# Kernel tuning notes

Measured on AMD Instinct MI355X. Metric: run time of the kernel, lower is better.

## Reference

```python
import jax, jax.numpy as jnp
import numpy as np

NT, NTRACES, NCH = 4096, 1024, 4


def setup_inputs() -> dict:
    key = jax.random.key(0)
    k1, k2 = jax.random.split(key)
    x = jax.random.normal(k1, (NT, NTRACES, NCH), dtype=jnp.float32)
    y = jax.random.normal(k2, (NT, NTRACES, NCH), dtype=jnp.float32)
    return {"x": x, "y": y}


def _quantiles(qs, cws, values):
    # quantile function of the discrete measure (values, weights with cumsum cws)
    # evaluated at cumulative-mass levels qs (POT solver_1d convention:
    # searchsorted side='left', clipped to valid index range).
    idx = jnp.clip(jnp.searchsorted(cws, qs, side="left"), 0, values.shape[0] - 1)
    return values[idx]


def _emd2_1d(xv, yv, w):
    # 1D EMD^2 (sqeuclidean ground metric, as in ot.emd2_1d defaults) between
    # atoms at positions xv with weights w and atoms at yv with weights w.
    ix = jnp.argsort(xv)
    iy = jnp.argsort(yv)
    xs, ys = xv[ix], yv[iy]            # sorted positions
    ca = jnp.cumsum(w[ix])             # cumulative source mass
    cb = jnp.cumsum(w[iy])             # cumulative target mass (equal total)
    qs = jnp.sort(jnp.concatenate([ca, cb]))  # merged mass breakpoints, (2*nt,)
    qx = _quantiles(qs, ca, xs)
    qy = _quantiles(qs, cb, ys)
    delta = jnp.diff(qs, prepend=0.0)  # mass in each segment
    return jnp.sum(delta * (qx - qy) ** 2)


def _sinkhorn_pair(xv, yv, t):
    # faithful to Sinkhorn._sinkhorn: clamp(min=0) -> cumsum -> divide by the
    # SUM of the cumsum (note: not the last element) -> 1D EMD with positions
    # (xv, yv) and weights t = arange(nt)  [positional args of ot.emd2_1d].
    xv = jnp.cumsum(jnp.clip(xv, 0.0))
    yv = jnp.cumsum(jnp.clip(yv, 0.0))
    xv = xv / jnp.sum(xv)
    yv = yv / jnp.sum(yv)
    return _emd2_1d(xv, yv, t)


def reference(x, y):
    nt = x.shape[0]
    t = jnp.arange(nt, dtype=jnp.float32)
    xf = x.reshape(nt, -1).T  # (ntraces*nchannels, nt)
    yf = y.reshape(nt, -1).T
    losses = jax.vmap(_sinkhorn_pair, in_axes=(0, 0, None))(xf, yf, t)
    return jnp.sum(losses)
```

## Files before the change

### kernel.cpp

```cpp
#include <hip/hip_runtime.h>


#define NT   4096
#define NP   4096
#define CH   64
#define LCH  64
#define BLK  256

__global__ __launch_bounds__(BLK) void p1_moments(
    const float* __restrict__ x, const float* __restrict__ y,
    float* __restrict__ aX, float* __restrict__ aY,
    float* __restrict__ uL, float* __restrict__ uM,
    float* __restrict__ pL, float* __restrict__ pM,
    float* __restrict__ pLL, float* __restrict__ pMM,
    float* __restrict__ pLM)
{
  const int pv = blockIdx.x * BLK + threadIdx.x;
  const int j  = blockIdx.y;
  const int t0 = j * LCH;
  const float2* xb = (const float2*)x + (size_t)t0 * (NP / 2) + pv;
  const float2* yb = (const float2*)y + (size_t)t0 * (NP / 2) + pv;

  float cx0 = 0.f, cx1 = 0.f, cy0 = 0.f, cy1 = 0.f;
  float uL0 = 0.f, uL1 = 0.f, uM0 = 0.f, uM1 = 0.f;
  float pL0 = 0.f, pL1 = 0.f, pM0 = 0.f, pM1 = 0.f;
  float pLL0 = 0.f, pLL1 = 0.f, pMM0 = 0.f, pMM1 = 0.f;
  float pLM0 = 0.f, pLM1 = 0.f;

#pragma unroll 8
  for (int i = 0; i < LCH; ++i) {
    const float2 xv = xb[(size_t)i * (NP / 2)];
    const float2 yv = yb[(size_t)i * (NP / 2)];
    const float t = (float)(t0 + i);

    const float lx0 = fmaxf(xv.x, 0.f), lx1 = fmaxf(xv.y, 0.f);
    const float ly0 = fmaxf(yv.x, 0.f), ly1 = fmaxf(yv.y, 0.f);

    cx0 += lx0; cy0 += ly0;
    const float tl0 = t * cx0, tm0 = t * cy0;
    pL0  += tl0;                  pM0  += tm0;
    pLL0 = fmaf(tl0, cx0, pLL0);  pMM0 = fmaf(tm0, cy0, pMM0);
    pLM0 = fmaf(tl0, cy0, pLM0);
    uL0  += cx0;                  uM0  += cy0;

    cx1 += lx1; cy1 += ly1;
    const float tl1 = t * cx1, tm1 = t * cy1;
    pL1  += tl1;                  pM1  += tm1;
    pLL1 = fmaf(tl1, cx1, pLL1);  pMM1 = fmaf(tm1, cy1, pMM1);
    pLM1 = fmaf(tl1, cy1, pLM1);
    uL1  += cx1;                  uM1  += cy1;
  }

  const size_t o2 = (size_t)j * (NP / 2) + pv;
  ((float2*)aX)[o2]  = make_float2(cx0, cx1);
  ((float2*)aY)[o2]  = make_float2(cy0, cy1);
  ((float2*)uL)[o2]  = make_float2(uL0, uL1);
  ((float2*)uM)[o2]  = make_float2(uM0, uM1);
  ((float2*)pL)[o2]  = make_float2(pL0, pL1);
  ((float2*)pM)[o2]  = make_float2(pM0, pM1);
  ((float2*)pLL)[o2] = make_float2(pLL0, pLL1);
  ((float2*)pMM)[o2] = make_float2(pMM0, pMM1);
  ((float2*)pLM)[o2] = make_float2(pLM0, pLM1);
}

__global__ __launch_bounds__(BLK) void p2_loss(
    const float* __restrict__ aX, const float* __restrict__ aY,
    const float* __restrict__ uL, const float* __restrict__ uM,
    const float* __restrict__ pL, const float* __restrict__ pM,
    const float* __restrict__ pLL, const float* __restrict__ pMM,
    const float* __restrict__ pLM,
    double* __restrict__ part)
{
  const int wave = threadIdx.x >> 6;
  const int lane = threadIdx.x & 63;
  const int p    = blockIdx.x * 4 + wave;
  const size_t o = (size_t)lane * NP + p;

  const double a  = (double)aX[o];
  const double b  = (double)aY[o];
  const double ul = (double)uL[o];
  const double um = (double)uM[o];

  double sx = a, sy = b;
  for (int d = 1; d < 64; d <<= 1) {
    const double tx = __shfl_up(sx, d, 64);
    const double ty = __shfl_up(sy, d, 64);
    if (lane >= d) { sx += tx; sy += ty; }
  }
  const double O = sx - a;
  const double P = sy - b;

  double vx = (double)LCH * O + ul;
  double vy = (double)LCH * P + um;
  for (int m = 32; m; m >>= 1) {
    vx += __shfl_xor(vx, m, 64);
    vy += __shfl_xor(vy, m, 64);
  }
  const double isx = 1.0 / vx;
  const double isy = 1.0 / vy;

  const double g   = isx * O - isy * P;
  const double Tj  = 4096.0 * (double)lane + 2016.0;
  const double sh  = isx * (double)pL[o] - isy * (double)pM[o];
  const double shh = isx * isx * (double)pLL[o]
                   - 2.0 * isx * isy * (double)pLM[o]
                   + isy * isy * (double)pMM[o];
  double loss = g * g * Tj + 2.0 * g * sh + shh;

  for (int m = 32; m; m >>= 1) loss += __shfl_xor(loss, m, 64);
  if (lane == 0) part[p] = loss;
}

__global__ __launch_bounds__(1024) void p3_final(
    const double* __restrict__ part, float* __restrict__ out)
{
  __shared__ double red[1024];
  double v = 0.0;
  for (int i = threadIdx.x; i < NP; i += 1024) v += part[i];
  red[threadIdx.x] = v;
  __syncthreads();
  for (int s = 512; s > 0; s >>= 1) {
    if (threadIdx.x < s) red[threadIdx.x] += red[threadIdx.x + s];
    __syncthreads();
  }
  if (threadIdx.x == 0) out[0] = (float)red[0];
}

extern "C" void kernel_launch(void* const* d_in, const int* in_sizes, int n_in,
                              void* d_out, int out_size, void* d_ws, size_t ws_size,
                              hipStream_t stream) {
  const float* x = (const float*)d_in[0];
  const float* y = (const float*)d_in[1];
  float* out = (float*)d_out;

  const size_t CNP = (size_t)CH * NP;
  char* ws = (char*)d_ws;
  float* aX  = (float*)ws; ws += CNP * sizeof(float);
  float* aY  = (float*)ws; ws += CNP * sizeof(float);
  float* uL  = (float*)ws; ws += CNP * sizeof(float);
  float* uM  = (float*)ws; ws += CNP * sizeof(float);
  float* pL  = (float*)ws; ws += CNP * sizeof(float);
  float* pM  = (float*)ws; ws += CNP * sizeof(float);
  float* pLL = (float*)ws; ws += CNP * sizeof(float);
  float* pMM = (float*)ws; ws += CNP * sizeof(float);
  float* pLM = (float*)ws; ws += CNP * sizeof(float);
  double* part = (double*)ws; ws += (size_t)NP * sizeof(double);

  dim3 g1((NP / 2) / BLK, CH);
  p1_moments<<<g1, BLK, 0, stream>>>(x, y, aX, aY, uL, uM, pL, pM, pLL, pMM, pLM);
  p2_loss<<<NP / 4, BLK, 0, stream>>>(aX, aY, uL, uM, pL, pM, pLL, pMM, pLM, part);
  p3_final<<<1, 1024, 0, stream>>>(part, out);
}
```

Baseline: 166.0 us.

## Split time axis into 256 chunks with float4 loads and two-level scan

Adds a new path that splits the time axis into 256 chunks of 16 steps. Each thread handles four series with float4 loads in blocks of 1024 threads, which gives more parallel work in the first pass. The second kernel now does a serial-plus-shared-memory two-level prefix scan over the 256 chunk moments for 64 series per block, and the final reduction shrinks to a single 64-lane wave. The new path needs four times the workspace for the intermediate moment arrays, which adds memory traffic. The old layout is kept as a fallback when the workspace is too small.

```diff
diff --git a/kernel.cpp b/kernel.cpp
--- a/kernel.cpp
+++ b/kernel.cpp
@@ -1,13 +1,15 @@
 #include <hip/hip_runtime.h>
 
 
-#define NT   4096
-#define NP   4096
-#define CH   64
-#define LCH  64
-#define BLK  256
-
-__global__ __launch_bounds__(BLK) void p1_moments(
+#define NT 4096
+#define NP 4096
+
+#define A_CH  256
+#define A_LCH 16
+#define A_B1  1024
+#define A_B2  512
+
+__global__ __launch_bounds__(A_B1, 4) void p1_moments_a(
     const float* __restrict__ x, const float* __restrict__ y,
     float* __restrict__ aX, float* __restrict__ aY,
     float* __restrict__ uL, float* __restrict__ uM,
@@ -15,9 +17,138 @@
     float* __restrict__ pLL, float* __restrict__ pMM,
     float* __restrict__ pLM)
 {
-  const int pv = blockIdx.x * BLK + threadIdx.x;
+  const int tid = threadIdx.x;
+  const int j   = blockIdx.x;
+  const int t0  = j * A_LCH;
+  const float4* xb = (const float4*)x + (size_t)t0 * (NP / 4) + tid;
+  const float4* yb = (const float4*)y + (size_t)t0 * (NP / 4) + tid;
+
+  float cx[4] = {0,0,0,0}, cy[4] = {0,0,0,0};
+  float auL[4] = {0,0,0,0}, auM[4] = {0,0,0,0};
+  float apL[4] = {0,0,0,0}, apM[4] = {0,0,0,0};
+  float aLL[4] = {0,0,0,0}, aMM[4] = {0,0,0,0}, aLM[4] = {0,0,0,0};
+
+#pragma unroll 4
+  for (int i = 0; i < A_LCH; ++i) {
+    const float4 xv = xb[(size_t)i * (NP / 4)];
+    const float4 yv = yb[(size_t)i * (NP / 4)];
+    const float t = (float)(t0 + i);
+    const float lx[4] = {xv.x, xv.y, xv.z, xv.w};
+    const float ly[4] = {yv.x, yv.y, yv.z, yv.w};
+#pragma unroll
+    for (int k = 0; k < 4; ++k) {
+      const float sx = fmaxf(lx[k], 0.f);
+      const float sy = fmaxf(ly[k], 0.f);
+      cx[k] += sx;  cy[k] += sy;
+      const float tl = t * cx[k], tm = t * cy[k];
+      apL[k] += tl;                  apM[k] += tm;
+      aLL[k] = fmaf(tl, cx[k], aLL[k]);
+      aMM[k] = fmaf(tm, cy[k], aMM[k]);
+      aLM[k] = fmaf(tl, cy[k], aLM[k]);
+      auL[k] += cx[k];               auM[k] += cy[k];
+    }
+  }
+
+  const size_t o = (size_t)j * NP;
+  ((float4*)(aX  + o))[tid] = make_float4(cx[0],  cx[1],  cx[2],  cx[3]);
+  ((float4*)(aY  + o))[tid] = make_float4(cy[0],  cy[1],  cy[2],  cy[3]);
+  ((float4*)(uL  + o))[tid] = make_float4(auL[0], auL[1], auL[2], auL[3]);
+  ((float4*)(uM  + o))[tid] = make_float4(auM[0], auM[1], auM[2], auM[3]);
+  ((float4*)(pL  + o))[tid] = make_float4(apL[0], apL[1], apL[2], apL[3]);
+  ((float4*)(pM  + o))[tid] = make_float4(apM[0], apM[1], apM[2], apM[3]);
+  ((float4*)(pLL + o))[tid] = make_float4(aLL[0], aLL[1], aLL[2], aLL[3]);
+  ((float4*)(pMM + o))[tid] = make_float4(aMM[0], aMM[1], aMM[2], aMM[3]);
+  ((float4*)(pLM + o))[tid] = make_float4(aLM[0], aLM[1], aLM[2], aLM[3]);
+}
+
+__global__ __launch_bounds__(A_B2) void p2_loss_a(
+    const float* __restrict__ aX, const float* __restrict__ aY,
+    const float* __restrict__ uL, const float* __restrict__ uM,
+    const float* __restrict__ pL, const float* __restrict__ pM,
+    const float* __restrict__ pLL, const float* __restrict__ pMM,
+    const float* __restrict__ pLM,
+    double* __restrict__ part)
+{
+  const int lane = threadIdx.x & 63;
+  const int g    = threadIdx.x >> 6;
+  const int p    = blockIdx.x * 64 + lane;
+  const int j0   = g * 32;
+
+  double ox = 0, oy = 0, s1x = 0, s1y = 0;
+#pragma unroll 4
+  for (int jj = 0; jj < 32; ++jj) {
+    const size_t off = (size_t)(j0 + jj) * NP + p;
+    s1x += (double)A_LCH * ox + (double)uL[off];
+    s1y += (double)A_LCH * oy + (double)uM[off];
+    ox += (double)aX[off];  oy += (double)aY[off];
+  }
+
+  __shared__ double Axs[8][64], Ays[8][64], Pxs[8][64], Pys[8][64];
+  Axs[g][lane] = ox;  Ays[g][lane] = oy;
+  Pxs[g][lane] = s1x; Pys[g][lane] = s1y;
+  __syncthreads();
+
+  double Qx = 0, Qy = 0, Sx = 0, Sy = 0, Qx_own = 0, Qy_own = 0;
+#pragma unroll
+  for (int gg = 0; gg < 8; ++gg) {
+    if (gg == g) { Qx_own = Qx; Qy_own = Qy; }
+    Sx += 512.0 * Qx + Pxs[gg][lane];
+    Sy += 512.0 * Qy + Pys[gg][lane];
+    Qx += Axs[gg][lane];
+    Qy += Ays[gg][lane];
+  }
+  const double isx = 1.0 / Sx, isy = 1.0 / Sy;
+
+  double O = Qx_own, P = Qy_own, loss = 0;
+#pragma unroll 4
+  for (int jj = 0; jj < 32; ++jj) {
+    const int jr = j0 + jj;
+    const size_t off = (size_t)jr * NP + p;
+    const double gg = isx * O - isy * P;
+    const double Tj = 256.0 * (double)jr + 120.0;
+    const double sh  = isx * (double)pL[off] - isy * (double)pM[off];
+    const double shh = isx * isx * (double)pLL[off]
+                     - 2.0 * isx * isy * (double)pLM[off]
+                     + isy * isy * (double)pMM[off];
+    loss += gg * gg * Tj + 2.0 * gg * sh + shh;
+    O += (double)aX[off];  P += (double)aY[off];
+  }
+
+  for (int m = 32; m; m >>= 1) loss += __shfl_xor(loss, m, 64);
+  __shared__ double wred[8];
+  if (lane == 0) wred[g] = loss;
+  __syncthreads();
+  if (threadIdx.x == 0) {
+    double v = 0;
+#pragma unroll
+    for (int i = 0; i < 8; ++i) v += wred[i];
+    part[blockIdx.x] = v;
+  }
+}
+
+__global__ __launch_bounds__(64) void p3_final_a(
+    const double* __restrict__ part, float* __restrict__ out)
+{
+  double v = part[threadIdx.x];
+  for (int m = 32; m; m >>= 1) v += __shfl_xor(v, m, 64);
+  if (threadIdx.x == 0) out[0] = (float)v;
+}
+
+#define B_CH  64
+#define B_LCH 64
+#define B_BLK 256
+
+__global__ __launch_bounds__(B_BLK) void p1_moments_b(
+    const float* __restrict__ x, const float* __restrict__ y,
+    float* __restrict__ aX, float* __restrict__ aY,
+    float* __restrict__ uL, float* __restrict__ uM,
+    float* __restrict__ pL, float* __restrict__ pM,
+    float* __restrict__ pLL, float* __restrict__ pMM,
+    float* __restrict__ pLM)
+{
+  const int pv = blockIdx.x * B_BLK + threadIdx.x;
   const int j  = blockIdx.y;
-  const int t0 = j * LCH;
+  const int t0 = j * B_LCH;
   const float2* xb = (const float2*)x + (size_t)t0 * (NP / 2) + pv;
   const float2* yb = (const float2*)y + (size_t)t0 * (NP / 2) + pv;
 
@@ -28,7 +159,7 @@
   float pLM0 = 0.f, pLM1 = 0.f;
 
 #pragma unroll 8
-  for (int i = 0; i < LCH; ++i) {
+  for (int i = 0; i < B_LCH; ++i) {
     const float2 xv = xb[(size_t)i * (NP / 2)];
     const float2 yv = yb[(size_t)i * (NP / 2)];
     const float t = (float)(t0 + i);
@@ -63,7 +194,7 @@
   ((float2*)pLM)[o2] = make_float2(pLM0, pLM1);
 }
 
-__global__ __launch_bounds__(BLK) void p2_loss(
+__global__ __launch_bounds__(B_BLK) void p2_loss_b(
     const float* __restrict__ aX, const float* __restrict__ aY,
     const float* __restrict__ uL, const float* __restrict__ uM,
     const float* __restrict__ pL, const float* __restrict__ pM,
@@ -90,8 +221,8 @@
   const double O = sx - a;
   const double P = sy - b;
 
-  double vx = (double)LCH * O + ul;
-  double vy = (double)LCH * P + um;
+  double vx = (double)B_LCH * O + ul;
+  double vy = (double)B_LCH * P + um;
   for (int m = 32; m; m >>= 1) {
     vx += __shfl_xor(vx, m, 64);
     vy += __shfl_xor(vy, m, 64);
@@ -111,7 +242,7 @@
   if (lane == 0) part[p] = loss;
 }
 
-__global__ __launch_bounds__(1024) void p3_final(
+__global__ __launch_bounds__(1024) void p3_final_b(
     const double* __restrict__ part, float* __restrict__ out)
 {
   __shared__ double red[1024];
@@ -133,21 +264,43 @@
   const float* y = (const float*)d_in[1];
   float* out = (float*)d_out;
 
-  const size_t CNP = (size_t)CH * NP;
-  char* ws = (char*)d_ws;
-  float* aX  = (float*)ws; ws += CNP * sizeof(float);
-  float* aY  = (float*)ws; ws += CNP * sizeof(float);
-  float* uL  = (float*)ws; ws += CNP * sizeof(float);
-  float* uM  = (float*)ws; ws += CNP * sizeof(float);
-  float* pL  = (float*)ws; ws += CNP * sizeof(float);
-  float* pM  = (float*)ws; ws += CNP * sizeof(float);
-  float* pLL = (float*)ws; ws += CNP * sizeof(float);
-  float* pMM = (float*)ws; ws += CNP * sizeof(float);
-  float* pLM = (float*)ws; ws += CNP * sizeof(float);
-  double* part = (double*)ws; ws += (size_t)NP * sizeof(double);
-
-  dim3 g1((NP / 2) / BLK, CH);
-  p1_moments<<<g1, BLK, 0, stream>>>(x, y, aX, aY, uL, uM, pL, pM, pLL, pMM, pLM);
-  p2_loss<<<NP / 4, BLK, 0, stream>>>(aX, aY, uL, uM, pL, pM, pLL, pMM, pLM, part);
-  p3_final<<<1, 1024, 0, stream>>>(part, out);
-}
+  const size_t cnpA = (size_t)A_CH * NP;
+  const size_t needA = 9 * cnpA * sizeof(float)
+                     + (size_t)(NP / 64) * sizeof(double) + 256;
+
+  if (ws_size >= needA) {
+    char* ws = (char*)d_ws;
+    float* aX  = (float*)ws; ws += cnpA * sizeof(float);
+    float* aY  = (float*)ws; ws += cnpA * sizeof(float);
+    float* uLp = (float*)ws; ws += cnpA * sizeof(float);
+    float* uMp = (float*)ws; ws += cnpA * sizeof(float);
+    float* pLp = (float*)ws; ws += cnpA * sizeof(float);
+    float* pMp = (float*)ws; ws += cnpA * sizeof(float);
+    float* pLLp = (float*)ws; ws += cnpA * sizeof(float);
+    float* pMMp = (float*)ws; ws += cnpA * sizeof(float);
+    float* pLMp = (float*)ws; ws += cnpA * sizeof(float);
+    double* part = (double*)ws;
+
+    p1_moments_a<<<A_CH, A_B1, 0, stream>>>(x, y, aX, aY, uLp, uMp, pLp, pMp, pLLp, pMMp, pLMp);
+    p2_loss_a<<<NP / 64, A_B2, 0, stream>>>(aX, aY, uLp, uMp, pLp, pMp, pLLp, pMMp, pLMp, part);
+    p3_final_a<<<1, 64, 0, stream>>>(part, out);
+  } else {
+    const size_t cnpB = (size_t)B_CH * NP;
+    char* ws = (char*)d_ws;
+    float* aX  = (float*)ws; ws += cnpB * sizeof(float);
+    float* aY  = (float*)ws; ws += cnpB * sizeof(float);
+    float* uLp = (float*)ws; ws += cnpB * sizeof(float);
+    float* uMp = (float*)ws; ws += cnpB * sizeof(float);
+    float* pLp = (float*)ws; ws += cnpB * sizeof(float);
+    float* pMp = (float*)ws; ws += cnpB * sizeof(float);
+    float* pLLp = (float*)ws; ws += cnpB * sizeof(float);
+    float* pMMp = (float*)ws; ws += cnpB * sizeof(float);
+    float* pLMp = (float*)ws; ws += cnpB * sizeof(float);
+    double* part = (double*)ws;
+
+    dim3 g1((NP / 2) / B_BLK, B_CH);
+    p1_moments_b<<<g1, B_BLK, 0, stream>>>(x, y, aX, aY, uLp, uMp, pLp, pMp, pLLp, pMMp, pLMp);
+    p2_loss_b<<<NP / 4, B_BLK, 0, stream>>>(aX, aY, uLp, uMp, pLp, pMp, pLLp, pMMp, pLMp, part);
+    p3_final_b<<<1, 1024, 0, stream>>>(part, out);
+  }
+}
```

Result: slower. 196.6 us (+18.5%).

## Split time into more, shorter chunks with one column per thread

Applied to the files above, without the earlier changes.

The first pass now uses 128 time chunks of 32 steps instead of 64 chunks of 64, and each thread handles one column with scalar loads instead of a float2 pair. Loads are batched in groups of 8 ahead of the compute, and launch bounds request higher occupancy. This gives more blocks and more parallel memory traffic to hide latency on the bandwidth-bound input read. The second pass is reworked so each lane combines two chunks, which doubles the intermediate workspace traffic and the per-lane work there.

```diff
diff --git a/kernel.cpp b/kernel.cpp
--- a/kernel.cpp
+++ b/kernel.cpp
@@ -3,11 +3,11 @@
 
 #define NT   4096
 #define NP   4096
-#define CH   64
-#define LCH  64
+#define CH   128
+#define LCH  32
 #define BLK  256
 
-__global__ __launch_bounds__(BLK) void p1_moments(
+__global__ __launch_bounds__(BLK, 8) void p1_moments(
     const float* __restrict__ x, const float* __restrict__ y,
     float* __restrict__ aX, float* __restrict__ aY,
     float* __restrict__ uL, float* __restrict__ uM,
@@ -15,52 +15,41 @@
     float* __restrict__ pLL, float* __restrict__ pMM,
     float* __restrict__ pLM)
 {
-  const int pv = blockIdx.x * BLK + threadIdx.x;
+  const int p  = blockIdx.x * BLK + threadIdx.x;
   const int j  = blockIdx.y;
   const int t0 = j * LCH;
-  const float2* xb = (const float2*)x + (size_t)t0 * (NP / 2) + pv;
-  const float2* yb = (const float2*)y + (size_t)t0 * (NP / 2) + pv;
+  const float* xp = x + (size_t)t0 * NP + p;
+  const float* yp = y + (size_t)t0 * NP + p;
 
-  float cx0 = 0.f, cx1 = 0.f, cy0 = 0.f, cy1 = 0.f;
-  float uL0 = 0.f, uL1 = 0.f, uM0 = 0.f, uM1 = 0.f;
-  float pL0 = 0.f, pL1 = 0.f, pM0 = 0.f, pM1 = 0.f;
-  float pLL0 = 0.f, pLL1 = 0.f, pMM0 = 0.f, pMM1 = 0.f;
-  float pLM0 = 0.f, pLM1 = 0.f;
+  float c_x = 0.f, c_y = 0.f;
+  float uLa = 0.f, uMa = 0.f, pLa = 0.f, pMa = 0.f;
+  float LLa = 0.f, MMa = 0.f, LMa = 0.f;
 
-#pragma unroll 8
-  for (int i = 0; i < LCH; ++i) {
-    const float2 xv = xb[(size_t)i * (NP / 2)];
-    const float2 yv = yb[(size_t)i * (NP / 2)];
-    const float t = (float)(t0 + i);
-
-    const float lx0 = fmaxf(xv.x, 0.f), lx1 = fmaxf(xv.y, 0.f);
-    const float ly0 = fmaxf(yv.x, 0.f), ly1 = fmaxf(yv.y, 0.f);
-
-    cx0 += lx0; cy0 += ly0;
-    const float tl0 = t * cx0, tm0 = t * cy0;
-    pL0  += tl0;                  pM0  += tm0;
-    pLL0 = fmaf(tl0, cx0, pLL0);  pMM0 = fmaf(tm0, cy0, pMM0);
-    pLM0 = fmaf(tl0, cy0, pLM0);
-    uL0  += cx0;                  uM0  += cy0;
-
-    cx1 += lx1; cy1 += ly1;
-    const float tl1 = t * cx1, tm1 = t * cy1;
-    pL1  += tl1;                  pM1  += tm1;
-    pLL1 = fmaf(tl1, cx1, pLL1);  pMM1 = fmaf(tm1, cy1, pMM1);
-    pLM1 = fmaf(tl1, cy1, pLM1);
-    uL1  += cx1;                  uM1  += cy1;
+  for (int g = 0; g < LCH / 8; ++g) {
+    float xs[8], ys[8];
+#pragma unroll
+    for (int i = 0; i < 8; ++i) {
+      xs[i] = xp[(size_t)(g * 8 + i) * NP];
+      ys[i] = yp[(size_t)(g * 8 + i) * NP];
+    }
+#pragma unroll
+    for (int i = 0; i < 8; ++i) {
+      const float t = (float)(t0 + g * 8 + i);
+      c_x += fmaxf(xs[i], 0.f);
+      c_y += fmaxf(ys[i], 0.f);
+      const float tl = t * c_x, tm = t * c_y;
+      pLa += tl;                  pMa += tm;
+      LLa = fmaf(tl, c_x, LLa);   MMa = fmaf(tm, c_y, MMa);
+      LMa = fmaf(tl, c_y, LMa);
+      uLa += c_x;                 uMa += c_y;
+    }
   }
 
-  const size_t o2 = (size_t)j * (NP / 2) + pv;
-  ((float2*)aX)[o2]  = make_float2(cx0, cx1);
-  ((float2*)aY)[o2]  = make_float2(cy0, cy1);
-  ((float2*)uL)[o2]  = make_float2(uL0, uL1);
-  ((float2*)uM)[o2]  = make_float2(uM0, uM1);
-  ((float2*)pL)[o2]  = make_float2(pL0, pL1);
-  ((float2*)pM)[o2]  = make_float2(pM0, pM1);
-  ((float2*)pLL)[o2] = make_float2(pLL0, pLL1);
-  ((float2*)pMM)[o2] = make_float2(pMM0, pMM1);
-  ((float2*)pLM)[o2] = make_float2(pLM0, pLM1);
+  const size_t o = (size_t)j * NP + p;
+  aX[o]  = c_x;  aY[o]  = c_y;
+  uL[o]  = uLa;  uM[o]  = uMa;
+  pL[o]  = pLa;  pM[o]  = pMa;
+  pLL[o] = LLa;  pMM[o] = MMa;  pLM[o] = LMa;
 }
 
 __global__ __launch_bounds__(BLK) void p2_loss(
@@ -74,24 +63,29 @@
   const int wave = threadIdx.x >> 6;
   const int lane = threadIdx.x & 63;
   const int p    = blockIdx.x * 4 + wave;
-  const size_t o = (size_t)lane * NP + p;
+  const int j0   = 2 * lane;
+  const size_t o0 = (size_t)j0 * NP + p;
+  const size_t o1 = o0 + NP;
 
-  const double a  = (double)aX[o];
-  const double b  = (double)aY[o];
-  const double ul = (double)uL[o];
-  const double um = (double)uM[o];
+  const double a0 = (double)aX[o0], a1 = (double)aX[o1];
+  const double b0 = (double)aY[o0], b1 = (double)aY[o1];
+  const double ul0 = (double)uL[o0], ul1 = (double)uL[o1];
+  const double um0 = (double)uM[o0], um1 = (double)uM[o1];
 
-  double sx = a, sy = b;
+  const double sA = a0 + a1, sB = b0 + b1;
+  double ix = sA, iy = sB;
   for (int d = 1; d < 64; d <<= 1) {
-    const double tx = __shfl_up(sx, d, 64);
-    const double ty = __shfl_up(sy, d, 64);
-    if (lane >= d) { sx += tx; sy += ty; }
+    const double tx = __shfl_up(ix, d, 64);
+    const double ty = __shfl_up(iy, d, 64);
+    if (lane >= d) { ix += tx; iy += ty; }
   }
-  const double O = sx - a;
-  const double P = sy - b;
+  const double O0 = ix - sA;
+  const double P0 = iy - sB;
+  const double O1 = O0 + a0;
+  const double P1 = P0 + b0;
 
-  double vx = (double)LCH * O + ul;
-  double vy = (double)LCH * P + um;
+  double vx = (double)LCH * (O0 + O1) + ul0 + ul1;
+  double vy = (double)LCH * (P0 + P1) + um0 + um1;
   for (int m = 32; m; m >>= 1) {
     vx += __shfl_xor(vx, m, 64);
     vy += __shfl_xor(vy, m, 64);
@@ -99,13 +93,25 @@
   const double isx = 1.0 / vx;
   const double isy = 1.0 / vy;
 
-  const double g   = isx * O - isy * P;
-  const double Tj  = 4096.0 * (double)lane + 2016.0;
-  const double sh  = isx * (double)pL[o] - isy * (double)pM[o];
-  const double shh = isx * isx * (double)pLL[o]
-                   - 2.0 * isx * isy * (double)pLM[o]
-                   + isy * isy * (double)pMM[o];
-  double loss = g * g * Tj + 2.0 * g * sh + shh;
+  double loss = 0.0;
+  {
+    const double g   = isx * O0 - isy * P0;
+    const double Tj  = 1024.0 * (double)j0 + 496.0;
+    const double sh  = isx * (double)pL[o0] - isy * (double)pM[o0];
+    const double shh = isx * isx * (double)pLL[o0]
+                     - 2.0 * isx * isy * (double)pLM[o0]
+                     + isy * isy * (double)pMM[o0];
+    loss += g * g * Tj + 2.0 * g * sh + shh;
+  }
+  {
+    const double g   = isx * O1 - isy * P1;
+    const double Tj  = 1024.0 * (double)(j0 + 1) + 496.0;
+    const double sh  = isx * (double)pL[o1] - isy * (double)pM[o1];
+    const double shh = isx * isx * (double)pLL[o1]
+                     - 2.0 * isx * isy * (double)pLM[o1]
+                     + isy * isy * (double)pMM[o1];
+    loss += g * g * Tj + 2.0 * g * sh + shh;
+  }
 
   for (int m = 32; m; m >>= 1) loss += __shfl_xor(loss, m, 64);
   if (lane == 0) part[p] = loss;
@@ -137,17 +143,17 @@
   char* ws = (char*)d_ws;
   float* aX  = (float*)ws; ws += CNP * sizeof(float);
   float* aY  = (float*)ws; ws += CNP * sizeof(float);
-  float* uL  = (float*)ws; ws += CNP * sizeof(float);
-  float* uM  = (float*)ws; ws += CNP * sizeof(float);
-  float* pL  = (float*)ws; ws += CNP * sizeof(float);
-  float* pM  = (float*)ws; ws += CNP * sizeof(float);
-  float* pLL = (float*)ws; ws += CNP * sizeof(float);
-  float* pMM = (float*)ws; ws += CNP * sizeof(float);
-  float* pLM = (float*)ws; ws += CNP * sizeof(float);
+  float* uLp = (float*)ws; ws += CNP * sizeof(float);
+  float* uMp = (float*)ws; ws += CNP * sizeof(float);
+  float* pLp = (float*)ws; ws += CNP * sizeof(float);
+  float* pMp = (float*)ws; ws += CNP * sizeof(float);
+  float* pLLp = (float*)ws; ws += CNP * sizeof(float);
+  float* pMMp = (float*)ws; ws += CNP * sizeof(float);
+  float* pLMp = (float*)ws; ws += CNP * sizeof(float);
   double* part = (double*)ws; ws += (size_t)NP * sizeof(double);
 
-  dim3 g1((NP / 2) / BLK, CH);
-  p1_moments<<<g1, BLK, 0, stream>>>(x, y, aX, aY, uL, uM, pL, pM, pLL, pMM, pLM);
-  p2_loss<<<NP / 4, BLK, 0, stream>>>(aX, aY, uL, uM, pL, pM, pLL, pMM, pLM, part);
+  dim3 g1(NP / BLK, CH);
+  p1_moments<<<g1, BLK, 0, stream>>>(x, y, aX, aY, uLp, uMp, pLp, pMp, pLLp, pMMp, pLMp);
+  p2_loss<<<NP / 4, BLK, 0, stream>>>(aX, aY, uLp, uMp, pLp, pMp, pLLp, pMMp, pLMp, part);
   p3_final<<<1, 1024, 0, stream>>>(part, out);
 }
```

Result: slower. 190.2 us (+14.6%).
